# Performance work log

Measured on AMD Instinct MI355X. Metric: run time of the kernel, lower is better.

Reference implementation:

```python
import jax, jax.numpy as jnp
import numpy as np

IN_DIM = 5000
OUT_DIM = 30
K = 50
BATCH = 16384


def setup_inputs() -> dict:
    key = jax.random.key(0)
    ks = jax.random.split(key, 8)
    return {
        "x": jax.random.normal(ks[0], (BATCH, IN_DIM), dtype=jnp.float32),
        "logits": jax.random.normal(ks[1], (IN_DIM,), dtype=jnp.float32),
        "W1": jax.random.normal(ks[2], (IN_DIM, 32), dtype=jnp.float32) * (1.0 / np.sqrt(IN_DIM)),
        "b1": jax.random.normal(ks[3], (32,), dtype=jnp.float32) * 0.01,
        "W2": jax.random.normal(ks[4], (32, 16), dtype=jnp.float32) * (1.0 / np.sqrt(32)),
        "b2": jax.random.normal(ks[5], (16,), dtype=jnp.float32) * 0.01,
        "W3": jax.random.normal(ks[6], (16, OUT_DIM), dtype=jnp.float32) * (1.0 / np.sqrt(16)),
        "b3": jax.random.normal(ks[7], (OUT_DIM,), dtype=jnp.float32) * 0.01,
        "epoch": 10,
        "total_epochs": 100,
    }


def reference(x, logits, W1, b1, W2, b2, W3, b3, epoch, total_epochs):
    # Eval path (training=False): top-k one-hot mask over the learned logits.
    # indices of top-k logits -> k-hot mask of shape [in_dim]
    _, idx = jax.lax.top_k(logits, K)                 # [K]
    mask = jnp.zeros_like(logits).at[idx].set(1.0)    # [in_dim], k-hot
    xm = mask * x                                      # [B, in_dim] gated input
    h = jax.nn.relu(xm @ W1 + b1)                      # [B, 32]
    h = jax.nn.relu(h @ W2 + b2)                       # [B, 16]
    out = h @ W3 + b3                                  # [B, out_dim]
    return out, mask
```

## Files before the change

kernel.cpp:

```cpp
#include <hip/hip_runtime.h>
#include <hip/hip_bf16.h>

#define N_IN 5000
#define K_SEL 50
#define B_ROWS 16384
#define OUT_D 30

__global__ __launch_bounds__(1024) void topk_mask_kernel(
    const float* __restrict__ logits,
    float* __restrict__ mask,
    int* __restrict__ idx_out)
{
    __shared__ unsigned int keys[N_IN];
    __shared__ unsigned int hist[256];
    __shared__ unsigned int s_prefix;
    __shared__ int s_remaining;
    __shared__ int s_eq_ticket;
    __shared__ int s_sel;

    const int tid = threadIdx.x;

    for (int i = tid; i < N_IN; i += 1024) {
        unsigned int b = __float_as_uint(logits[i]);
        keys[i] = (b & 0x80000000u) ? ~b : (b | 0x80000000u);
        mask[i] = 0.0f;
    }
    if (tid == 0) { s_prefix = 0u; s_remaining = K_SEL; s_eq_ticket = 0; s_sel = 0; }
    __syncthreads();

    for (int shift = 24; shift >= 0; shift -= 8) {
        for (int i = tid; i < 256; i += 1024) hist[i] = 0u;
        __syncthreads();
        const unsigned int pref = s_prefix;
        const int hi = shift + 8;
        for (int i = tid; i < N_IN; i += 1024) {
            unsigned int k = keys[i];
            bool cand = (hi >= 32) ? true : ((k >> hi) == pref);
            if (cand) atomicAdd(&hist[(k >> shift) & 0xFFu], 1u);
        }
        __syncthreads();
        if (tid == 0) {
            int rem = s_remaining;
            int c = 0;
            int d = 255;
            for (;; d--) {
                int c2 = c + (int)hist[d];
                if (c2 >= rem || d == 0) {
                    s_remaining = rem - c;
                    s_prefix = (pref << 8) | (unsigned int)d;
                    break;
                }
                c = c2;
            }
        }
        __syncthreads();
    }

    const unsigned int KT = s_prefix;
    const int rem = s_remaining;

    for (int i = tid; i < N_IN; i += 1024) {
        unsigned int k = keys[i];
        bool sel = false;
        if (k > KT) {
            sel = true;
        } else if (k == KT) {
            int t = atomicAdd(&s_eq_ticket, 1);
            if (t < rem) sel = true;
        }
        if (sel) {
            int slot = atomicAdd(&s_sel, 1);
            idx_out[slot] = i;
            mask[i] = 1.0f;
        }
    }
}

__global__ __launch_bounds__(64) void gated_mlp_kernel(
    const float* __restrict__ x,
    const float* __restrict__ W1,
    const float* __restrict__ b1,
    const float* __restrict__ W2,
    const float* __restrict__ b2,
    const float* __restrict__ W3,
    const float* __restrict__ b3,
    const int* __restrict__ idx,
    float* __restrict__ out)
{
    __shared__ float sW1[K_SEL * 32];
    __shared__ float sW2[32 * 16];
    __shared__ float sW3[16 * OUT_D];
    __shared__ float sb1[32];
    __shared__ float sb2[16];
    __shared__ float sb3[OUT_D];
    __shared__ int   sidx[K_SEL];

    const int tid = threadIdx.x;

    if (tid < K_SEL) sidx[tid] = idx[tid];
    for (int t = tid; t < K_SEL * 32; t += 64) {
        int k = t >> 5;
        int j = t & 31;
        sW1[t] = W1[(size_t)idx[k] * 32 + j];
    }
    for (int t = tid; t < 32 * 16; t += 64) sW2[t] = W2[t];
    for (int t = tid; t < 16 * OUT_D; t += 64) sW3[t] = W3[t];
    if (tid < 32) sb1[tid] = b1[tid];
    if (tid < 16) sb2[tid] = b2[tid];
    if (tid < OUT_D) sb3[tid] = b3[tid];
    __syncthreads();

    const int r = blockIdx.x * 64 + tid;
    const float* __restrict__ xrow = x + (size_t)r * N_IN;

    float xv[K_SEL];
#pragma unroll
    for (int k = 0; k < K_SEL; k++) {
        xv[k] = xrow[sidx[k]];
    }

    float acc[32];
#pragma unroll
    for (int j = 0; j < 32; j++) acc[j] = sb1[j];
#pragma unroll
    for (int k = 0; k < K_SEL; k++) {
        float xk = xv[k];
#pragma unroll
        for (int j = 0; j < 32; j++) acc[j] = fmaf(xk, sW1[k * 32 + j], acc[j]);
    }

    float h2[16];
#pragma unroll
    for (int j = 0; j < 16; j++) h2[j] = sb2[j];
#pragma unroll
    for (int i = 0; i < 32; i++) {
        float a = fmaxf(acc[i], 0.0f);
#pragma unroll
        for (int j = 0; j < 16; j++) h2[j] = fmaf(a, sW2[i * 16 + j], h2[j]);
    }

    float o[OUT_D];
#pragma unroll
    for (int j = 0; j < OUT_D; j++) o[j] = sb3[j];
#pragma unroll
    for (int i = 0; i < 16; i++) {
        float a = fmaxf(h2[i], 0.0f);
#pragma unroll
        for (int j = 0; j < OUT_D; j++) o[j] = fmaf(a, sW3[i * OUT_D + j], o[j]);
    }

    float* __restrict__ orow = out + (size_t)r * OUT_D;
#pragma unroll
    for (int j = 0; j < OUT_D; j++) orow[j] = o[j];
}

extern "C" void kernel_launch(void* const* d_in, const int* in_sizes, int n_in,
                              void* d_out, int out_size, void* d_ws, size_t ws_size,
                              hipStream_t stream) {
    const float* x      = (const float*)d_in[0];
    const float* logits = (const float*)d_in[1];
    const float* W1     = (const float*)d_in[2];
    const float* b1     = (const float*)d_in[3];
    const float* W2     = (const float*)d_in[4];
    const float* b2     = (const float*)d_in[5];
    const float* W3     = (const float*)d_in[6];
    const float* b3     = (const float*)d_in[7];

    float* out  = (float*)d_out;
    float* mask = out + (size_t)B_ROWS * OUT_D;
    int*   idx  = (int*)d_ws;

    topk_mask_kernel<<<1, 1024, 0, stream>>>(logits, mask, idx);
    gated_mlp_kernel<<<256, 64, 0, stream>>>(x, W1, b1, W2, b2, W3, b3, idx, out);
}
```

Baseline: 450.3 us.

## Use register binary-search top-k and cooperative gather with staged coalesced output

Result: faster. 432.0 us (-4.0%).

```diff
diff --git a/kernel.cpp b/kernel.cpp
--- a/kernel.cpp
+++ b/kernel.cpp
@@ -11,62 +11,68 @@
     float* __restrict__ mask,
     int* __restrict__ idx_out)
 {
-    __shared__ unsigned int keys[N_IN];
-    __shared__ unsigned int hist[256];
-    __shared__ unsigned int s_prefix;
-    __shared__ int s_remaining;
-    __shared__ int s_eq_ticket;
-    __shared__ int s_sel;
+    __shared__ unsigned int s_cnt[34];
+    __shared__ int s_tick, s_sel;
 
-    const int tid = threadIdx.x;
+    const int tid  = threadIdx.x;
+    const int lane = tid & 63;
 
-    for (int i = tid; i < N_IN; i += 1024) {
-        unsigned int b = __float_as_uint(logits[i]);
-        keys[i] = (b & 0x80000000u) ? ~b : (b | 0x80000000u);
-        mask[i] = 0.0f;
+    if (tid < 34) s_cnt[tid] = 0u;
+    if (tid == 40) { s_tick = 0; }
+    if (tid == 41) { s_sel = 0; }
+
+    unsigned int key[5];
+#pragma unroll
+    for (int j = 0; j < 5; j++) {
+        int i = tid + j * 1024;
+        if (i < N_IN) {
+            unsigned int b = __float_as_uint(logits[i]);
+            key[j] = (b & 0x80000000u) ? ~b : (b | 0x80000000u);
+            mask[i] = 0.0f;
+        } else {
+            key[j] = 0u;
+        }
     }
-    if (tid == 0) { s_prefix = 0u; s_remaining = K_SEL; s_eq_ticket = 0; s_sel = 0; }
     __syncthreads();
 
-    for (int shift = 24; shift >= 0; shift -= 8) {
-        for (int i = tid; i < 256; i += 1024) hist[i] = 0u;
+    unsigned int lo = 0u, hi = 0xFFFFFFFFu;
+    for (int iter = 0; iter < 32; iter++) {
+        if (lo >= hi) break;
+        unsigned int mid = lo + ((hi - lo) >> 1) + 1u;
+        unsigned int c = 0;
+#pragma unroll
+        for (int j = 0; j < 5; j++) c += (key[j] >= mid) ? 1u : 0u;
+#pragma unroll
+        for (int off = 32; off > 0; off >>= 1) c += __shfl_down(c, off, 64);
+        if (lane == 0) atomicAdd(&s_cnt[iter], c);
         __syncthreads();
-        const unsigned int pref = s_prefix;
-        const int hi = shift + 8;
-        for (int i = tid; i < N_IN; i += 1024) {
-            unsigned int k = keys[i];
-            bool cand = (hi >= 32) ? true : ((k >> hi) == pref);
-            if (cand) atomicAdd(&hist[(k >> shift) & 0xFFu], 1u);
-        }
-        __syncthreads();
-        if (tid == 0) {
-            int rem = s_remaining;
-            int c = 0;
-            int d = 255;
-            for (;; d--) {
-                int c2 = c + (int)hist[d];
-                if (c2 >= rem || d == 0) {
-                    s_remaining = rem - c;
-                    s_prefix = (pref << 8) | (unsigned int)d;
-                    break;
-                }
-                c = c2;
-            }
-        }
-        __syncthreads();
+        unsigned int cnt = s_cnt[iter];
+        if (cnt >= (unsigned)K_SEL) lo = mid; else hi = mid - 1u;
     }
+    const unsigned int KT = lo;
 
-    const unsigned int KT = s_prefix;
-    const int rem = s_remaining;
+    {
+        unsigned int c = 0;
+#pragma unroll
+        for (int j = 0; j < 5; j++) c += (key[j] > KT) ? 1u : 0u;
+#pragma unroll
+        for (int off = 32; off > 0; off >>= 1) c += __shfl_down(c, off, 64);
+        if (lane == 0) atomicAdd(&s_cnt[33], c);
+    }
+    __syncthreads();
+    const int rem = K_SEL - (int)s_cnt[33];
 
-    for (int i = tid; i < N_IN; i += 1024) {
-        unsigned int k = keys[i];
+#pragma unroll
+    for (int j = 0; j < 5; j++) {
+        int i = tid + j * 1024;
+        if (i >= N_IN) continue;
+        unsigned int k = key[j];
         bool sel = false;
         if (k > KT) {
             sel = true;
         } else if (k == KT) {
-            int t = atomicAdd(&s_eq_ticket, 1);
-            if (t < rem) sel = true;
+            int t = atomicAdd(&s_tick, 1);
+            sel = (t < rem);
         }
         if (sel) {
             int slot = atomicAdd(&s_sel, 1);
@@ -76,7 +82,7 @@
     }
 }
 
-__global__ __launch_bounds__(64) void gated_mlp_kernel(
+__global__ __launch_bounds__(256) void gated_mlp_kernel(
     const float* __restrict__ x,
     const float* __restrict__ W1,
     const float* __restrict__ b1,
@@ -87,6 +93,7 @@
     const int* __restrict__ idx,
     float* __restrict__ out)
 {
+    __shared__ float xs[64 * 51];
     __shared__ float sW1[K_SEL * 32];
     __shared__ float sW2[32 * 16];
     __shared__ float sW3[16 * OUT_D];
@@ -98,60 +105,73 @@
     const int tid = threadIdx.x;
 
     if (tid < K_SEL) sidx[tid] = idx[tid];
-    for (int t = tid; t < K_SEL * 32; t += 64) {
-        int k = t >> 5;
-        int j = t & 31;
-        sW1[t] = W1[(size_t)idx[k] * 32 + j];
+    for (int e = tid; e < K_SEL * 32; e += 256) {
+        int k = e >> 5, j = e & 31;
+        sW1[e] = W1[(size_t)idx[k] * 32 + j];
     }
-    for (int t = tid; t < 32 * 16; t += 64) sW2[t] = W2[t];
-    for (int t = tid; t < 16 * OUT_D; t += 64) sW3[t] = W3[t];
+    for (int e = tid; e < 32 * 16; e += 256) sW2[e] = W2[e];
+    for (int e = tid; e < 16 * OUT_D; e += 256) sW3[e] = W3[e];
     if (tid < 32) sb1[tid] = b1[tid];
     if (tid < 16) sb2[tid] = b2[tid];
     if (tid < OUT_D) sb3[tid] = b3[tid];
     __syncthreads();
 
-    const int r = blockIdx.x * 64 + tid;
-    const float* __restrict__ xrow = x + (size_t)r * N_IN;
+    const int r  = tid >> 2;
+    const int q  = tid & 3;
+    const int row = blockIdx.x * 64 + r;
+    const float* __restrict__ xrow = x + (size_t)row * N_IN;
+    for (int k = q; k < K_SEL; k += 4) {
+        xs[r * 51 + k] = xrow[sidx[k]];
+    }
+    __syncthreads();
 
-    float xv[K_SEL];
+    float so_local[OUT_D];
+    if (tid < 64) {
+        const float* xr = &xs[tid * 51];
+
+        float acc[32];
 #pragma unroll
-    for (int k = 0; k < K_SEL; k++) {
-        xv[k] = xrow[sidx[k]];
+        for (int j = 0; j < 32; j++) acc[j] = sb1[j];
+#pragma unroll
+        for (int k = 0; k < K_SEL; k++) {
+            float xk = xr[k];
+#pragma unroll
+            for (int j = 0; j < 32; j++) acc[j] = fmaf(xk, sW1[k * 32 + j], acc[j]);
+        }
+
+        float h2[16];
+#pragma unroll
+        for (int j = 0; j < 16; j++) h2[j] = sb2[j];
+#pragma unroll
+        for (int i = 0; i < 32; i++) {
+            float a = fmaxf(acc[i], 0.0f);
+#pragma unroll
+            for (int j = 0; j < 16; j++) h2[j] = fmaf(a, sW2[i * 16 + j], h2[j]);
+        }
+
+#pragma unroll
+        for (int j = 0; j < OUT_D; j++) so_local[j] = sb3[j];
+#pragma unroll
+        for (int i = 0; i < 16; i++) {
+            float a = fmaxf(h2[i], 0.0f);
+#pragma unroll
+            for (int j = 0; j < OUT_D; j++) so_local[j] = fmaf(a, sW3[i * OUT_D + j], so_local[j]);
+        }
     }
+    __syncthreads();
 
-    float acc[32];
+    float* so = xs;
+    if (tid < 64) {
 #pragma unroll
-    for (int j = 0; j < 32; j++) acc[j] = sb1[j];
-#pragma unroll
-    for (int k = 0; k < K_SEL; k++) {
-        float xk = xv[k];
-#pragma unroll
-        for (int j = 0; j < 32; j++) acc[j] = fmaf(xk, sW1[k * 32 + j], acc[j]);
+        for (int j = 0; j < OUT_D; j++) so[tid * OUT_D + j] = so_local[j];
     }
+    __syncthreads();
 
-    float h2[16];
-#pragma unroll
-    for (int j = 0; j < 16; j++) h2[j] = sb2[j];
-#pragma unroll
-    for (int i = 0; i < 32; i++) {
-        float a = fmaxf(acc[i], 0.0f);
-#pragma unroll
-        for (int j = 0; j < 16; j++) h2[j] = fmaf(a, sW2[i * 16 + j], h2[j]);
+    float4* out4 = (float4*)(out + (size_t)blockIdx.x * 64 * OUT_D);
+    const float4* so4 = (const float4*)so;
+    for (int e = tid; e < (64 * OUT_D) / 4; e += 256) {
+        out4[e] = so4[e];
     }
-
-    float o[OUT_D];
-#pragma unroll
-    for (int j = 0; j < OUT_D; j++) o[j] = sb3[j];
-#pragma unroll
-    for (int i = 0; i < 16; i++) {
-        float a = fmaxf(h2[i], 0.0f);
-#pragma unroll
-        for (int j = 0; j < OUT_D; j++) o[j] = fmaf(a, sW3[i * OUT_D + j], o[j]);
-    }
-
-    float* __restrict__ orow = out + (size_t)r * OUT_D;
-#pragma unroll
-    for (int j = 0; j < OUT_D; j++) orow[j] = o[j];
 }
 
 extern "C" void kernel_launch(void* const* d_in, const int* in_sizes, int n_in,
@@ -171,5 +191,5 @@
     int*   idx  = (int*)d_ws;
 
     topk_mask_kernel<<<1, 1024, 0, stream>>>(logits, mask, idx);
-    gated_mlp_kernel<<<256, 64, 0, stream>>>(x, W1, b1, W2, b2, W3, b3, idx, out);
+    gated_mlp_kernel<<<256, 256, 0, stream>>>(x, W1, b1, W2, b2, W3, b3, idx, out);
 }
```
